# Optimization experiments

Measured on AMD Instinct MI355X. Metric: run time of the kernel, lower is better.

The kernel has to match this reference:

```python
import jax, jax.numpy as jnp
from jax import lax
import numpy as np

FEAT = 256
B = 16
T = 4096
BETA = 1.0


def setup_inputs() -> dict:
    key = jax.random.key(0)
    k0, k1, k2 = jax.random.split(key, 3)
    encoder_outputs = jax.random.normal(k0, (B, T, FEAT), dtype=jnp.float32)
    # Conv1d weight: (out_ch, in_ch, kernel)
    conv_w = jax.random.normal(k1, (FEAT, FEAT, 5), dtype=jnp.float32) * 0.02
    conv_b = jnp.zeros((FEAT,), dtype=jnp.float32)
    lin_w = jax.random.normal(k2, (FEAT, 1), dtype=jnp.float32) * 0.05
    lin_b = jnp.zeros((1,), dtype=jnp.float32)
    return {"encoder_outputs": encoder_outputs, "conv_w": conv_w,
            "conv_b": conv_b, "lin_w": lin_w, "lin_b": lin_b}


def _alphas(x, conv_w, conv_b, lin_w, lin_b):
    # x: [B, T, D] -> alphas [B, T]
    xc = jnp.transpose(x, (0, 2, 1))  # NCH
    y = lax.conv_general_dilated(xc, conv_w, window_strides=(1,),
                                 padding='SAME',
                                 dimension_numbers=('NCH', 'OIH', 'NCH'))
    y = y + conv_b[None, :, None]
    y = jnp.transpose(y, (0, 2, 1))  # [B, T, D]
    return jax.nn.sigmoid(y @ lin_w + lin_b)[..., 0]  # [B, T]


def _cif_single(alpha, h, beta):
    # alpha: [T], h: [T, D]  integrate-and-fire scan
    D = h.shape[-1]
    Tlen = alpha.shape[0]

    def step(carry, inp):
        acc, hacc = carry
        a, hu = inp
        acc_new = acc + a
        fire = acc_new >= beta
        a1 = 1.0 - acc          # mass to complete current segment
        c = hacc + a1 * hu      # emitted segment vector (if fired)
        a2 = a - a1             # leftover mass starting next segment
        acc_out = jnp.where(fire, a2, acc_new)
        hacc_out = jnp.where(fire, a2 * hu, hacc + a * hu)
        return (acc_out, hacc_out), (fire, jnp.where(fire, c, jnp.zeros_like(c)))

    init = (jnp.zeros((), h.dtype), jnp.zeros((D,), h.dtype))
    (acc_f, hacc_f), (fires, cs) = lax.scan(step, init, (alpha, h))

    # pack fired emissions densely; non-fired steps scatter into dump slot Tlen
    idx = jnp.cumsum(fires.astype(jnp.int32)) - 1
    idx = jnp.where(fires, idx, Tlen)
    out = jnp.zeros((Tlen + 1, D), h.dtype).at[idx].add(cs)[:Tlen]
    n = fires.sum().astype(jnp.int32)
    # if no segment fired, emit the final accumulator (torch: c=[h_accum[-1]])
    out = out.at[0].set(jnp.where(n == 0, hacc_f, out[0]))
    n = jnp.maximum(n, 1)
    return out, n


def reference(encoder_outputs, conv_w, conv_b, lin_w, lin_b):
    alphas = _alphas(encoder_outputs, conv_w, conv_b, lin_w, lin_b)  # [B, T]
    out_c, len_tensor = jax.vmap(lambda a, h: _cif_single(a, h, BETA))(
        alphas, encoder_outputs)
    return out_c, len_tensor
```

## Files before the change

### kernel.cpp

```cpp
#include <hip/hip_runtime.h>
#include <math.h>

#define FEAT 256
#define NB   16
#define TLEN 4096
#define NROWS (NB * TLEN)

#define OFF_WEFF 0
#define OFF_BEFF 1280
#define OFF_P    2048
#define OFF_W1   (OFF_P + 5 * NROWS)
#define OFF_W2   (OFF_W1 + NROWS)
#define OFF_FPOS (OFF_W2 + NROWS)
#define OFF_NF   (OFF_FPOS + NROWS)

__global__ __launch_bounds__(256) void weff_kernel(
    const float* __restrict__ conv_w, const float* __restrict__ conv_b,
    const float* __restrict__ lin_w, const float* __restrict__ lin_b,
    float* __restrict__ ws) {
  if (blockIdx.x < 5) {
    int idx = blockIdx.x * 256 + threadIdx.x;
    int i = idx / 5, k = idx - i * 5;
    float acc = 0.f;
    for (int o = 0; o < FEAT; ++o)
      acc = fmaf(conv_w[o * (FEAT * 5) + idx], lin_w[o], acc);
    ws[OFF_WEFF + k * FEAT + i] = acc;
  } else {
    __shared__ float red[256];
    red[threadIdx.x] = conv_b[threadIdx.x] * lin_w[threadIdx.x];
    __syncthreads();
    for (int s = 128; s > 0; s >>= 1) {
      if (threadIdx.x < s) red[threadIdx.x] += red[threadIdx.x + s];
      __syncthreads();
    }
    if (threadIdx.x == 0) ws[OFF_BEFF] = red[0] + lin_b[0];
  }
}

__global__ __launch_bounds__(256) void pdot_kernel(
    const float* __restrict__ x, float* __restrict__ ws) {
  int gtid = blockIdx.x * 256 + threadIdx.x;
  int row  = gtid >> 6;
  int lane = gtid & 63;
  float4 xv = *(const float4*)(x + (size_t)row * FEAT + lane * 4);
  float p[5];
#pragma unroll
  for (int k = 0; k < 5; ++k) {
    float4 w4 = *(const float4*)(ws + OFF_WEFF + k * FEAT + lane * 4);
    p[k] = fmaf(xv.x, w4.x, fmaf(xv.y, w4.y, fmaf(xv.z, w4.z, xv.w * w4.w)));
#pragma unroll
    for (int off = 32; off; off >>= 1) p[k] += __shfl_xor(p[k], off);
  }
  if (lane == 0) {
#pragma unroll
    for (int k = 0; k < 5; ++k) ws[OFF_P + (size_t)k * NROWS + row] = p[k];
  }
}

__global__ __launch_bounds__(256) void scan_kernel(
    float* __restrict__ ws, float* __restrict__ out) {
  const int b = blockIdx.x;
  __shared__ float  s_alpha[TLEN];
  __shared__ double s_S[TLEN];
  __shared__ double s_part[256];
  const float b_eff = ws[OFF_BEFF];

  for (int j = 0; j < TLEN / 256; ++j) {
    int t = j * 256 + threadIdx.x;
    float z = b_eff;
#pragma unroll
    for (int k = 0; k < 5; ++k) {
      int tt = t + k - 2;
      if (tt >= 0 && tt < TLEN) z += ws[OFF_P + (size_t)k * NROWS + b * TLEN + tt];
    }
    s_alpha[t] = 1.f / (1.f + expf(-z));
  }
  __syncthreads();

  const int base = threadIdx.x * 16;
  double run = 0.0;
#pragma unroll
  for (int r = 0; r < 16; ++r) { run += (double)s_alpha[base + r]; s_S[base + r] = run; }
  s_part[threadIdx.x] = run;
  __syncthreads();
  for (int s = 1; s < 256; s <<= 1) {
    double add = (threadIdx.x >= s) ? s_part[threadIdx.x - s] : 0.0;
    __syncthreads();
    if (threadIdx.x >= s) s_part[threadIdx.x] += add;
    __syncthreads();
  }
  double offset = threadIdx.x ? s_part[threadIdx.x - 1] : 0.0;

  double Sprev = offset;
  double Fprev = floor(Sprev);
  float* w1 = ws + OFF_W1 + b * TLEN;
  float* w2 = ws + OFF_W2 + b * TLEN;
  int* fpos = (int*)ws + OFF_FPOS + b * TLEN;
#pragma unroll
  for (int r = 0; r < 16; ++r) {
    int t = base + r;
    double St = offset + s_S[t];
    double Ft = floor(St);
    w1[t] = (float)(fmin(St, Fprev + 1.0) - Sprev);
    if (Ft > Fprev) {
      w2[t] = (float)(St - Ft);
      fpos[(int)Ft - 1] = t;
    }
    Sprev = St; Fprev = Ft;
  }
  if (threadIdx.x == 255) {
    int n = (int)Fprev;
    ((int*)ws)[OFF_NF + b] = n;
    out[(size_t)NROWS * FEAT + b] = (float)(n > 0 ? n : 1);
  }
}

__global__ __launch_bounds__(256) void emit_kernel(
    const float* __restrict__ x, const float* __restrict__ ws,
    float* __restrict__ out) {
  int gtid = blockIdx.x * 256 + threadIdx.x;
  int row  = gtid >> 6;
  int lane = gtid & 63;
  int b = row >> 12;
  int j = row & (TLEN - 1);
  int n = ((const int*)ws)[OFF_NF + b];
  int keep = n > 0 ? n : 1;
  float4 acc = make_float4(0.f, 0.f, 0.f, 0.f);
  if (j < keep) {
    const int* fpos = (const int*)ws + OFF_FPOS + b * TLEN;
    int t_lo = j ? fpos[j - 1] : 0;
    int t_hi = (j < n) ? fpos[j] : TLEN - 1;
    const float* w1 = ws + OFF_W1 + b * TLEN;
    const float* w2 = ws + OFF_W2 + b * TLEN;
    for (int t = t_lo; t <= t_hi; ++t) {
      float w = (j && t == t_lo) ? w2[t] : w1[t];
      float4 xv = *(const float4*)(x + ((size_t)b * TLEN + t) * FEAT + lane * 4);
      acc.x = fmaf(w, xv.x, acc.x);
      acc.y = fmaf(w, xv.y, acc.y);
      acc.z = fmaf(w, xv.z, acc.z);
      acc.w = fmaf(w, xv.w, acc.w);
    }
  }
  *(float4*)(out + (size_t)row * FEAT + lane * 4) = acc;
}

extern "C" void kernel_launch(void* const* d_in, const int* in_sizes, int n_in,
                              void* d_out, int out_size, void* d_ws, size_t ws_size,
                              hipStream_t stream) {
  const float* x      = (const float*)d_in[0];
  const float* conv_w = (const float*)d_in[1];
  const float* conv_b = (const float*)d_in[2];
  const float* lin_w  = (const float*)d_in[3];
  const float* lin_b  = (const float*)d_in[4];
  float* out = (float*)d_out;
  float* ws  = (float*)d_ws;

  hipLaunchKernelGGL(weff_kernel, dim3(6), dim3(256), 0, stream,
                     conv_w, conv_b, lin_w, lin_b, ws);
  hipLaunchKernelGGL(pdot_kernel, dim3(NROWS / 4), dim3(256), 0, stream, x, ws);
  hipLaunchKernelGGL(scan_kernel, dim3(NB), dim3(256), 0, stream, ws, out);
  hipLaunchKernelGGL(emit_kernel, dim3(NROWS / 4), dim3(256), 0, stream, x, ws, out);
}
```

Before: 168.8 us.

## Split weight folding across blocks, restructure pdot rows, drop shared prefix array

The serial 256-step weight-folding loop is split into 40 blocks that each write a partial sum, and a second small kernel adds the partials, which adds one launch. pdot now assigns 8 lanes per row and loops over the feature dimension, so each wave handles 8 rows and the shuffle reduction shrinks to three steps. The scan kernel no longer stores a double prefix array in shared memory; it recomputes local running sums from padded alpha storage to avoid bank conflicts and reduce LDS use.

```diff
diff --git a/kernel.cpp b/kernel.cpp
--- a/kernel.cpp
+++ b/kernel.cpp
@@ -13,17 +13,30 @@
 #define OFF_W2   (OFF_W1 + NROWS)
 #define OFF_FPOS (OFF_W2 + NROWS)
 #define OFF_NF   (OFF_FPOS + NROWS)
+#define OFF_PART (OFF_NF + 16)
 
-__global__ __launch_bounds__(256) void weff_kernel(
-    const float* __restrict__ conv_w, const float* __restrict__ conv_b,
-    const float* __restrict__ lin_w, const float* __restrict__ lin_b,
+__global__ __launch_bounds__(256) void weff1_kernel(
+    const float* __restrict__ conv_w, const float* __restrict__ lin_w,
     float* __restrict__ ws) {
+  int ob = blockIdx.x % 5, oc = blockIdx.x / 5;
+  int idx = ob * 256 + threadIdx.x;
+  float acc = 0.f;
+  int o0 = oc * 32;
+#pragma unroll 8
+  for (int o = o0; o < o0 + 32; ++o)
+    acc = fmaf(conv_w[o * (FEAT * 5) + idx], lin_w[o], acc);
+  ws[OFF_PART + oc * 1280 + idx] = acc;
+}
+
+__global__ __launch_bounds__(256) void weff2_kernel(
+    const float* __restrict__ conv_b, const float* __restrict__ lin_w,
+    const float* __restrict__ lin_b, float* __restrict__ ws) {
   if (blockIdx.x < 5) {
     int idx = blockIdx.x * 256 + threadIdx.x;
+    float acc = 0.f;
+#pragma unroll
+    for (int c = 0; c < 8; ++c) acc += ws[OFF_PART + c * 1280 + idx];
     int i = idx / 5, k = idx - i * 5;
-    float acc = 0.f;
-    for (int o = 0; o < FEAT; ++o)
-      acc = fmaf(conv_w[o * (FEAT * 5) + idx], lin_w[o], acc);
     ws[OFF_WEFF + k * FEAT + i] = acc;
   } else {
     __shared__ float red[256];
@@ -39,31 +52,42 @@
 
 __global__ __launch_bounds__(256) void pdot_kernel(
     const float* __restrict__ x, float* __restrict__ ws) {
-  int gtid = blockIdx.x * 256 + threadIdx.x;
-  int row  = gtid >> 6;
-  int lane = gtid & 63;
-  float4 xv = *(const float4*)(x + (size_t)row * FEAT + lane * 4);
-  float p[5];
+  int tid  = threadIdx.x;
+  int wave = tid >> 6, l = tid & 63;
+  int row  = blockIdx.x * 32 + wave * 8 + (l >> 3);
+  int l8   = l & 7;
+  const float* xr = x + (size_t)row * FEAT + l8 * 4;
+  float p[5] = {0.f, 0.f, 0.f, 0.f, 0.f};
+#pragma unroll
+  for (int pass = 0; pass < 8; ++pass) {
+    float4 xv = *(const float4*)(xr + pass * 32);
+#pragma unroll
+    for (int k = 0; k < 5; ++k) {
+      float4 w4 = *(const float4*)(ws + OFF_WEFF + k * FEAT + pass * 32 + l8 * 4);
+      p[k] = fmaf(xv.x, w4.x, fmaf(xv.y, w4.y,
+              fmaf(xv.z, w4.z, fmaf(xv.w, w4.w, p[k]))));
+    }
+  }
 #pragma unroll
   for (int k = 0; k < 5; ++k) {
-    float4 w4 = *(const float4*)(ws + OFF_WEFF + k * FEAT + lane * 4);
-    p[k] = fmaf(xv.x, w4.x, fmaf(xv.y, w4.y, fmaf(xv.z, w4.z, xv.w * w4.w)));
-#pragma unroll
-    for (int off = 32; off; off >>= 1) p[k] += __shfl_xor(p[k], off);
+    p[k] += __shfl_xor(p[k], 1);
+    p[k] += __shfl_xor(p[k], 2);
+    p[k] += __shfl_xor(p[k], 4);
   }
-  if (lane == 0) {
+  if (l8 == 0) {
 #pragma unroll
     for (int k = 0; k < 5; ++k) ws[OFF_P + (size_t)k * NROWS + row] = p[k];
   }
 }
 
+#define PAD(t) ((t) + ((t) >> 4))
 __global__ __launch_bounds__(256) void scan_kernel(
     float* __restrict__ ws, float* __restrict__ out) {
   const int b = blockIdx.x;
-  __shared__ float  s_alpha[TLEN];
-  __shared__ double s_S[TLEN];
+  __shared__ float  s_alpha[TLEN + (TLEN >> 4)];
   __shared__ double s_part[256];
   const float b_eff = ws[OFF_BEFF];
+  const float* Pb = ws + OFF_P + (size_t)b * TLEN;
 
   for (int j = 0; j < TLEN / 256; ++j) {
     int t = j * 256 + threadIdx.x;
@@ -71,16 +95,16 @@
 #pragma unroll
     for (int k = 0; k < 5; ++k) {
       int tt = t + k - 2;
-      if (tt >= 0 && tt < TLEN) z += ws[OFF_P + (size_t)k * NROWS + b * TLEN + tt];
+      if (tt >= 0 && tt < TLEN) z += Pb[(size_t)k * NROWS + tt];
     }
-    s_alpha[t] = 1.f / (1.f + expf(-z));
+    s_alpha[PAD(t)] = 1.f / (1.f + expf(-z));
   }
   __syncthreads();
 
   const int base = threadIdx.x * 16;
   double run = 0.0;
 #pragma unroll
-  for (int r = 0; r < 16; ++r) { run += (double)s_alpha[base + r]; s_S[base + r] = run; }
+  for (int r = 0; r < 16; ++r) run += (double)s_alpha[PAD(base + r)];
   s_part[threadIdx.x] = run;
   __syncthreads();
   for (int s = 1; s < 256; s <<= 1) {
@@ -96,10 +120,12 @@
   float* w1 = ws + OFF_W1 + b * TLEN;
   float* w2 = ws + OFF_W2 + b * TLEN;
   int* fpos = (int*)ws + OFF_FPOS + b * TLEN;
+  double runl = 0.0;
 #pragma unroll
   for (int r = 0; r < 16; ++r) {
     int t = base + r;
-    double St = offset + s_S[t];
+    runl += (double)s_alpha[PAD(t)];
+    double St = offset + runl;
     double Ft = floor(St);
     w1[t] = (float)(fmin(St, Fprev + 1.0) - Sprev);
     if (Ft > Fprev) {
@@ -155,9 +181,11 @@
   float* out = (float*)d_out;
   float* ws  = (float*)d_ws;
 
-  hipLaunchKernelGGL(weff_kernel, dim3(6), dim3(256), 0, stream,
-                     conv_w, conv_b, lin_w, lin_b, ws);
-  hipLaunchKernelGGL(pdot_kernel, dim3(NROWS / 4), dim3(256), 0, stream, x, ws);
+  hipLaunchKernelGGL(weff1_kernel, dim3(40), dim3(256), 0, stream,
+                     conv_w, lin_w, ws);
+  hipLaunchKernelGGL(weff2_kernel, dim3(6), dim3(256), 0, stream,
+                     conv_b, lin_w, lin_b, ws);
+  hipLaunchKernelGGL(pdot_kernel, dim3(NROWS / 32), dim3(256), 0, stream, x, ws);
   hipLaunchKernelGGL(scan_kernel, dim3(NB), dim3(256), 0, stream, ws, out);
   hipLaunchKernelGGL(emit_kernel, dim3(NROWS / 4), dim3(256), 0, stream, x, ws, out);
 }
```

Result: faster. 165.4 us (-2.0%).
